# Performance work log

Measured on AMD Instinct MI355X. Metric: run time of the kernel, lower is better.

The kernel has to match this reference:

```python
import jax, jax.numpy as jnp
import numpy as np

N_NODES = 100000
N_EDGES = 3200000
R0, R1, R2, N1 = 16, 8, 16, 32


def setup_inputs() -> dict:
    key = jax.random.key(0)
    ks = jax.random.split(key, 12)
    x = jax.random.normal(ks[0], (N_NODES, R0), dtype=jnp.float32)
    edge_index = jax.random.randint(ks[1], (2, N_EDGES), 0, N_NODES, dtype=jnp.int64)
    s = 0.1
    return {
        "x": x,
        "edge_index": edge_index,
        # GraphConv 1: lin_rel (weight+bias) applied to aggregated neighbors, lin_root (no bias) to self
        "W_rel1": jax.random.normal(ks[2], (R0, R1), dtype=jnp.float32) * s,
        "b_rel1": jnp.zeros((R1,), dtype=jnp.float32),
        "W_root1": jax.random.normal(ks[3], (R0, R1), dtype=jnp.float32) * s,
        # GraphConv 2
        "W_rel2": jax.random.normal(ks[4], (R1, R2), dtype=jnp.float32) * s,
        "b_rel2": jnp.zeros((R2,), dtype=jnp.float32),
        "W_root2": jax.random.normal(ks[5], (R1, R2), dtype=jnp.float32) * s,
        # fc layers
        "W_fc1": jax.random.normal(ks[6], (R2, N1), dtype=jnp.float32) * s,
        "b_fc1": jnp.zeros((N1,), dtype=jnp.float32),
        "W_fc2": jax.random.normal(ks[7], (N1, 1), dtype=jnp.float32) * s,
        "b_fc2": jnp.zeros((1,), dtype=jnp.float32),
    }


def _graph_conv(x, src, dst, W_rel, b_rel, W_root):
    # GraphConv with aggr='add': out_i = lin_rel(sum_{j->i} x_j) + lin_root(x_i)
    agg = jax.ops.segment_sum(x[src], dst, num_segments=N_NODES)  # [N, d_in]
    return agg @ W_rel + b_rel + x @ W_root


def reference(x, edge_index,
              W_rel1, b_rel1, W_root1,
              W_rel2, b_rel2, W_root2,
              W_fc1, b_fc1, W_fc2, b_fc2):
    src, dst = edge_index[0], edge_index[1]
    h = jax.nn.relu(_graph_conv(x, src, dst, W_rel1, b_rel1, W_root1))
    h = jax.nn.relu(_graph_conv(h, src, dst, W_rel2, b_rel2, W_root2))
    h = jax.nn.relu(h @ W_fc1 + b_fc1)
    out = h @ W_fc2 + b_fc2  # [N, 1]
    return out - jnp.mean(out)
```

## Files before the change

### kernel.cpp

```cpp
#include <hip/hip_runtime.h>

#define NN 100000
#define NE 3200000
#define BSH 7
#define BNODES 128
#define NBUCK 782
#define BCAP 4800
#define BIN_CHUNK 8192
#define NBIN_BLOCKS ((NE + BIN_CHUNK - 1) / BIN_CHUNK)

#define S1 2097152.0f
#define S2 524288.0f
#define INV_S1 (1.0f / S1)
#define INV_S2 (1.0f / S2)

__global__ void node_layer1(const float* __restrict__ x,
                            const float* __restrict__ Wrel1,
                            const float* __restrict__ brel1,
                            const float* __restrict__ Wroot1,
                            int* __restrict__ y1q,
                            int* __restrict__ initq,
                            int* __restrict__ bucketCnt ) {
    __shared__ float sW[16 * 8];
    __shared__ float sR[16 * 8];
    __shared__ float sb[8];
    int t = threadIdx.x;
    if (t < 128) { sW[t] = Wrel1[t]; sR[t] = Wroot1[t]; }
    if (t < 8)   { sb[t] = brel1[t]; }
    if (blockIdx.x == 0) {
        for (int k = t; k < NBUCK + 1; k += 256) bucketCnt[k] = 0;
    }
    __syncthreads();

    int i = blockIdx.x * blockDim.x + t;
    if (i >= NN) return;

    const float4* xp = (const float4*)(x + (size_t)i * 16);
    float4 x0 = xp[0], x1 = xp[1], x2 = xp[2], x3 = xp[3];
    float xi[16] = {x0.x, x0.y, x0.z, x0.w, x1.x, x1.y, x1.z, x1.w,
                    x2.x, x2.y, x2.z, x2.w, x3.x, x3.y, x3.z, x3.w};

    float y[8], r[8];
#pragma unroll
    for (int j = 0; j < 8; ++j) { y[j] = 0.0f; r[j] = sb[j]; }
#pragma unroll
    for (int k = 0; k < 16; ++k) {
        float xv = xi[k];
#pragma unroll
        for (int j = 0; j < 8; ++j) {
            y[j] = fmaf(xv, sW[k * 8 + j], y[j]);
            r[j] = fmaf(xv, sR[k * 8 + j], r[j]);
        }
    }
    int4* yp = (int4*)(y1q + (size_t)i * 8);
    int4* ap = (int4*)(initq + (size_t)i * 8);
    int4 q0, q1, p0, p1;
    q0.x = __float2int_rn(y[0] * S1); q0.y = __float2int_rn(y[1] * S1);
    q0.z = __float2int_rn(y[2] * S1); q0.w = __float2int_rn(y[3] * S1);
    q1.x = __float2int_rn(y[4] * S1); q1.y = __float2int_rn(y[5] * S1);
    q1.z = __float2int_rn(y[6] * S1); q1.w = __float2int_rn(y[7] * S1);
    p0.x = __float2int_rn(r[0] * S1); p0.y = __float2int_rn(r[1] * S1);
    p0.z = __float2int_rn(r[2] * S1); p0.w = __float2int_rn(r[3] * S1);
    p1.x = __float2int_rn(r[4] * S1); p1.y = __float2int_rn(r[5] * S1);
    p1.z = __float2int_rn(r[6] * S1); p1.w = __float2int_rn(r[7] * S1);
    yp[0] = q0; yp[1] = q1;
    ap[0] = p0; ap[1] = p1;
}

__global__ __launch_bounds__(1024) void binning(const int* __restrict__ src,
                                                const int* __restrict__ dst,
                                                int* __restrict__ bucketCnt,
                                                int* __restrict__ bpay) {
    __shared__ int stage[BIN_CHUNK];
    __shared__ int hist[NBUCK];
    __shared__ int loff[NBUCK + 1];
    __shared__ int gbase[NBUCK];
    __shared__ int psum[1024];

    int t = threadIdx.x;
    int e0 = blockIdx.x * BIN_CHUNK;
    int nE = NE - e0; if (nE > BIN_CHUNK) nE = BIN_CHUNK;
    int nv = nE >> 2;

    if (t < NBUCK) hist[t] = 0;
    __syncthreads();

    const int4* dst4 = (const int4*)(dst + e0);
    const int4* src4 = (const int4*)(src + e0);

    for (int k = t; k < nv; k += 1024) {
        int4 d4 = dst4[k];
        atomicAdd(&hist[d4.x >> BSH], 1);
        atomicAdd(&hist[d4.y >> BSH], 1);
        atomicAdd(&hist[d4.z >> BSH], 1);
        atomicAdd(&hist[d4.w >> BSH], 1);
    }
    __syncthreads();

    int c = (t < NBUCK) ? hist[t] : 0;
    psum[t] = c;
    __syncthreads();
    for (int off = 1; off < 1024; off <<= 1) {
        int u = (t >= off) ? psum[t - off] : 0;
        __syncthreads();
        psum[t] += u;
        __syncthreads();
    }
    if (t < NBUCK) loff[t] = psum[t] - c;
    if (t == 0) loff[NBUCK] = nE;
    __syncthreads();

    if (t < NBUCK) {
        gbase[t] = c ? atomicAdd(&bucketCnt[t], c) : 0;
        hist[t] = loff[t];
    }
    __syncthreads();

    for (int k = t; k < nv; k += 1024) {
        int4 d4 = dst4[k];
        int4 s4 = src4[k];
        int b, r;
        b = d4.x >> BSH; r = atomicAdd(&hist[b], 1);
        stage[r] = ((d4.x & (BNODES - 1)) << 17) | s4.x;
        b = d4.y >> BSH; r = atomicAdd(&hist[b], 1);
        stage[r] = ((d4.y & (BNODES - 1)) << 17) | s4.y;
        b = d4.z >> BSH; r = atomicAdd(&hist[b], 1);
        stage[r] = ((d4.z & (BNODES - 1)) << 17) | s4.z;
        b = d4.w >> BSH; r = atomicAdd(&hist[b], 1);
        stage[r] = ((d4.w & (BNODES - 1)) << 17) | s4.w;
    }
    __syncthreads();

    for (int p = t; p < nE; p += 1024) {
        int lo = 0, hi = NBUCK - 1;
        while (lo < hi) {
            int mid = (lo + hi + 1) >> 1;
            if (loff[mid] <= p) lo = mid; else hi = mid - 1;
        }
        int ob = gbase[lo] + (p - loff[lo]);
        if (ob < BCAP) bpay[lo * BCAP + ob] = stage[p];
    }
}

__global__ __launch_bounds__(512, 6) void bucket_agg1(const int* __restrict__ bucketCnt,
                                                      const int* __restrict__ bpay,
                                                      const int* __restrict__ y1q,
                                                      int* __restrict__ h1q ) {
    __shared__ int qacc[BNODES * 8];
    int t = threadIdx.x;
    int b = blockIdx.x;
    int gb = b * BCAP;
    int fbase = b * (BNODES * 8);

    for (int k = t; k < BNODES * 8; k += 512) {
        int gi = fbase + k;
        qacc[k] = (gi < NN * 8) ? h1q[gi] : 0;
    }
    int C = bucketCnt[b]; if (C > BCAP) C = BCAP;
    __syncthreads();

    int f = t & 7, g = t >> 3;
    const int4* bp4 = (const int4*)(bpay + gb);
    int iters = C >> 9;
    for (int it = 0; it < iters; ++it) {
        int4 va = bp4[(it << 7) + (g << 1)];
        int4 vb = bp4[(it << 7) + (g << 1) + 1];
        int a0 = y1q[((va.x & 0x1FFFF) << 3) + f];
        int a1 = y1q[((va.y & 0x1FFFF) << 3) + f];
        int a2 = y1q[((va.z & 0x1FFFF) << 3) + f];
        int a3 = y1q[((va.w & 0x1FFFF) << 3) + f];
        int a4 = y1q[((vb.x & 0x1FFFF) << 3) + f];
        int a5 = y1q[((vb.y & 0x1FFFF) << 3) + f];
        int a6 = y1q[((vb.z & 0x1FFFF) << 3) + f];
        int a7 = y1q[((vb.w & 0x1FFFF) << 3) + f];
        atomicAdd(&qacc[((va.x >> 17) << 3) + f], a0);
        atomicAdd(&qacc[((va.y >> 17) << 3) + f], a1);
        atomicAdd(&qacc[((va.z >> 17) << 3) + f], a2);
        atomicAdd(&qacc[((va.w >> 17) << 3) + f], a3);
        atomicAdd(&qacc[((vb.x >> 17) << 3) + f], a4);
        atomicAdd(&qacc[((vb.y >> 17) << 3) + f], a5);
        atomicAdd(&qacc[((vb.z >> 17) << 3) + f], a6);
        atomicAdd(&qacc[((vb.w >> 17) << 3) + f], a7);
    }
    for (int e = (iters << 9) + g; e < C; e += 64) {
        int v = bpay[gb + e];
        int a = y1q[((v & 0x1FFFF) << 3) + f];
        atomicAdd(&qacc[((v >> 17) << 3) + f], a);
    }
    __syncthreads();

    for (int k = t; k < BNODES * 8; k += 512) {
        int gi = fbase + k;
        if (gi < NN * 8) {
            float h = (float)qacc[k] * INV_S1;
            h = h > 0.0f ? h : 0.0f;
            h1q[gi] = __float2int_rn(h * S2);
        }
    }
}

__global__ __launch_bounds__(512, 6) void bucket_agg2_tail(const int* __restrict__ bucketCnt,
                                                           const int* __restrict__ bpay,
                                                           const int* __restrict__ h1q,
                                                           const float* __restrict__ Wrel2,
                                                           const float* __restrict__ brel2,
                                                           const float* __restrict__ Wroot2,
                                                           const float* __restrict__ Wfc1,
                                                           const float* __restrict__ bfc1,
                                                           const float* __restrict__ Wfc2,
                                                           const float* __restrict__ bfc2,
                                                           float* __restrict__ out,
                                                           float* __restrict__ gsum) {
    __shared__ int qacc[BNODES * 8];
    __shared__ float sWrel2[128], sWroot2[128], sbrel2[16];
    __shared__ float sWfc1[512], sbfc1[32], sWfc2[32];
    __shared__ float sbfc2;
    __shared__ float wsum[8];

    int t = threadIdx.x;
    int b = blockIdx.x;
    int gb = b * BCAP;
    int n0 = b * BNODES;

    for (int k = t; k < BNODES * 8; k += 512) qacc[k] = 0;
    sWfc1[t] = Wfc1[t];
    if (t < 128) { sWrel2[t] = Wrel2[t]; sWroot2[t] = Wroot2[t]; }
    if (t >= 128 && t < 144) sbrel2[t - 128] = brel2[t - 128];
    if (t >= 192 && t < 224) { sbfc1[t - 192] = bfc1[t - 192]; sWfc2[t - 192] = Wfc2[t - 192]; }
    if (t == 256) sbfc2 = bfc2[0];
    int C = bucketCnt[b]; if (C > BCAP) C = BCAP;
    __syncthreads();

    int f = t & 7, g = t >> 3;
    const int4* bp4 = (const int4*)(bpay + gb);
    int iters = C >> 9;
    for (int it = 0; it < iters; ++it) {
        int4 va = bp4[(it << 7) + (g << 1)];
        int4 vb = bp4[(it << 7) + (g << 1) + 1];
        int a0 = h1q[((va.x & 0x1FFFF) << 3) + f];
        int a1 = h1q[((va.y & 0x1FFFF) << 3) + f];
        int a2 = h1q[((va.z & 0x1FFFF) << 3) + f];
        int a3 = h1q[((va.w & 0x1FFFF) << 3) + f];
        int a4 = h1q[((vb.x & 0x1FFFF) << 3) + f];
        int a5 = h1q[((vb.y & 0x1FFFF) << 3) + f];
        int a6 = h1q[((vb.z & 0x1FFFF) << 3) + f];
        int a7 = h1q[((vb.w & 0x1FFFF) << 3) + f];
        atomicAdd(&qacc[((va.x >> 17) << 3) + f], a0);
        atomicAdd(&qacc[((va.y >> 17) << 3) + f], a1);
        atomicAdd(&qacc[((va.z >> 17) << 3) + f], a2);
        atomicAdd(&qacc[((va.w >> 17) << 3) + f], a3);
        atomicAdd(&qacc[((vb.x >> 17) << 3) + f], a4);
        atomicAdd(&qacc[((vb.y >> 17) << 3) + f], a5);
        atomicAdd(&qacc[((vb.z >> 17) << 3) + f], a6);
        atomicAdd(&qacc[((vb.w >> 17) << 3) + f], a7);
    }
    for (int e = (iters << 9) + g; e < C; e += 64) {
        int v = bpay[gb + e];
        int a = h1q[((v & 0x1FFFF) << 3) + f];
        atomicAdd(&qacc[((v >> 17) << 3) + f], a);
    }
    __syncthreads();

    float o = 0.0f;
    int node = n0 + t;
    if (t < BNODES && node < NN) {
        const int4* hp = (const int4*)(h1q + (size_t)node * 8);
        int4 ha = hp[0], hb = hp[1];
        float h1v[8] = {ha.x * INV_S2, ha.y * INV_S2, ha.z * INV_S2, ha.w * INV_S2,
                        hb.x * INV_S2, hb.y * INV_S2, hb.z * INV_S2, hb.w * INV_S2};
        float s2[8];
#pragma unroll
        for (int j = 0; j < 8; ++j) s2[j] = (float)qacc[t * 8 + j] * INV_S2;

        float h2[16];
#pragma unroll
        for (int j = 0; j < 16; ++j) h2[j] = sbrel2[j];
#pragma unroll
        for (int k = 0; k < 8; ++k) {
            float sv = s2[k], hv = h1v[k];
#pragma unroll
            for (int j = 0; j < 16; ++j) {
                h2[j] = fmaf(sv, sWrel2[k * 16 + j], h2[j]);
                h2[j] = fmaf(hv, sWroot2[k * 16 + j], h2[j]);
            }
        }
#pragma unroll
        for (int j = 0; j < 16; ++j) h2[j] = h2[j] > 0.0f ? h2[j] : 0.0f;

        o = sbfc2;
#pragma unroll
        for (int m = 0; m < 32; ++m) {
            float a = sbfc1[m];
#pragma unroll
            for (int j = 0; j < 16; ++j) a = fmaf(h2[j], sWfc1[j * 32 + m], a);
            a = a > 0.0f ? a : 0.0f;
            o = fmaf(a, sWfc2[m], o);
        }
        out[node] = o;
    }

    float v = o;
#pragma unroll
    for (int off = 32; off > 0; off >>= 1) v += __shfl_down(v, off);
    int lane = t & 63, w = t >> 6;
    if (lane == 0) wsum[w] = v;
    __syncthreads();
    if (t == 0) {
        float s = 0.0f;
#pragma unroll
        for (int k = 0; k < 8; ++k) s += wsum[k];
        atomicAdd(gsum, s);
    }
}

__global__ void subtract_mean(float* __restrict__ out,
                              const float* __restrict__ gsum) {
    int i = blockIdx.x * blockDim.x + threadIdx.x;
    if (i < NN) out[i] -= (*gsum) * (1.0f / (float)NN);
}

extern "C" void kernel_launch(void* const* d_in, const int* in_sizes, int n_in,
                              void* d_out, int out_size, void* d_ws, size_t ws_size,
                              hipStream_t stream) {
    const float* x      = (const float*)d_in[0];
    const int*   ei     = (const int*)d_in[1];
    const float* Wrel1  = (const float*)d_in[2];
    const float* brel1  = (const float*)d_in[3];
    const float* Wroot1 = (const float*)d_in[4];
    const float* Wrel2  = (const float*)d_in[5];
    const float* brel2  = (const float*)d_in[6];
    const float* Wroot2 = (const float*)d_in[7];
    const float* Wfc1   = (const float*)d_in[8];
    const float* bfc1   = (const float*)d_in[9];
    const float* Wfc2   = (const float*)d_in[10];
    const float* bfc2   = (const float*)d_in[11];
    float* out = (float*)d_out;
    float* ws  = (float*)d_ws;

    int*   y1q       = (int*)ws;
    int*   h1q       = (int*)(ws + 800000);
    int*   bucketCnt = (int*)(ws + 1600000);
    float* gsum      = ws + 1600782;
    int*   bpay      = (int*)(ws + 1600783);

    const int* src = ei;
    const int* dst = ei + NE;

    node_layer1<<<(NN + 255) / 256, 256, 0, stream>>>(x, Wrel1, brel1, Wroot1,
                                                      y1q, h1q, bucketCnt);
    binning<<<NBIN_BLOCKS, 1024, 0, stream>>>(src, dst, bucketCnt, bpay);
    bucket_agg1<<<NBUCK, 512, 0, stream>>>(bucketCnt, bpay, y1q, h1q);
    bucket_agg2_tail<<<NBUCK, 512, 0, stream>>>(bucketCnt, bpay, h1q,
                                                Wrel2, brel2, Wroot2,
                                                Wfc1, bfc1, Wfc2, bfc2, out, gsum);
    subtract_mean<<<(NN + 255) / 256, 256, 0, stream>>>(out, gsum);
}
```

Baseline: 181.8 us.

## Fuse all GCN stages into one cooperative persistent kernel with grid syncs

After: 329.4 us. 81.2% more time.

```diff
diff --git a/kernel.cpp b/kernel.cpp
--- a/kernel.cpp
+++ b/kernel.cpp
@@ -1,4 +1,7 @@
 #include <hip/hip_runtime.h>
+#include <hip/hip_cooperative_groups.h>
+
+namespace cg = cooperative_groups;
 
 #define NN 100000
 #define NE 3200000
@@ -6,317 +9,308 @@
 #define BNODES 128
 #define NBUCK 782
 #define BCAP 4800
-#define BIN_CHUNK 8192
-#define NBIN_BLOCKS ((NE + BIN_CHUNK - 1) / BIN_CHUNK)
+#define NBLOCKS 256
+#define NTHREADS 1024
+#define CHUNK 12500
 
 #define S1 2097152.0f
 #define S2 524288.0f
 #define INV_S1 (1.0f / S1)
 #define INV_S2 (1.0f / S2)
 
-__global__ void node_layer1(const float* __restrict__ x,
-                            const float* __restrict__ Wrel1,
-                            const float* __restrict__ brel1,
-                            const float* __restrict__ Wroot1,
-                            int* __restrict__ y1q,
-                            int* __restrict__ initq,
-                            int* __restrict__ bucketCnt ) {
-    __shared__ float sW[16 * 8];
-    __shared__ float sR[16 * 8];
-    __shared__ float sb[8];
+struct BinSh {
+    int stage[CHUNK];
+    int hist[NBUCK];
+    int loff[NBUCK + 1];
+    int gbase[NBUCK];
+    int psum[NTHREADS];
+};
+struct ASh { float sW[128], sR[128], sb[8]; };
+struct AggSh {
+    int qacc[BNODES * 8];
+    float sWrel2[128], sWroot2[128], sbrel2[16];
+    float sWfc1[512], sbfc1[32], sWfc2[32], sbfc2;
+    float wsum[16];
+};
+union Sh { ASh a; BinSh bin; AggSh agg; };
+
+__global__ __launch_bounds__(NTHREADS, 4) void fused_gcn(
+    const float* __restrict__ x,
+    const int* __restrict__ src,
+    const int* __restrict__ dst,
+    const float* __restrict__ Wrel1, const float* __restrict__ brel1,
+    const float* __restrict__ Wroot1,
+    const float* __restrict__ Wrel2, const float* __restrict__ brel2,
+    const float* __restrict__ Wroot2,
+    const float* __restrict__ Wfc1, const float* __restrict__ bfc1,
+    const float* __restrict__ Wfc2, const float* __restrict__ bfc2,
+    int* __restrict__ y1q, int* __restrict__ h1q,
+    int* __restrict__ bucketCnt, float* __restrict__ gsum,
+    int* __restrict__ bpay, float* __restrict__ out)
+{
+    cg::grid_group grid = cg::this_grid();
+    __shared__ Sh sh;
     int t = threadIdx.x;
-    if (t < 128) { sW[t] = Wrel1[t]; sR[t] = Wroot1[t]; }
-    if (t < 8)   { sb[t] = brel1[t]; }
-    if (blockIdx.x == 0) {
-        for (int k = t; k < NBUCK + 1; k += 256) bucketCnt[k] = 0;
+    int blk = blockIdx.x;
+
+    if (t < 128) { sh.a.sW[t] = Wrel1[t]; sh.a.sR[t] = Wroot1[t]; }
+    if (t < 8)   sh.a.sb[t] = brel1[t];
+    if (blk == 0) {
+        for (int k = t; k < NBUCK; k += NTHREADS) bucketCnt[k] = 0;
+        if (t == 0) *gsum = 0.0f;
     }
     __syncthreads();
 
-    int i = blockIdx.x * blockDim.x + t;
-    if (i >= NN) return;
-
-    const float4* xp = (const float4*)(x + (size_t)i * 16);
-    float4 x0 = xp[0], x1 = xp[1], x2 = xp[2], x3 = xp[3];
-    float xi[16] = {x0.x, x0.y, x0.z, x0.w, x1.x, x1.y, x1.z, x1.w,
-                    x2.x, x2.y, x2.z, x2.w, x3.x, x3.y, x3.z, x3.w};
-
-    float y[8], r[8];
-#pragma unroll
-    for (int j = 0; j < 8; ++j) { y[j] = 0.0f; r[j] = sb[j]; }
-#pragma unroll
-    for (int k = 0; k < 16; ++k) {
-        float xv = xi[k];
-#pragma unroll
-        for (int j = 0; j < 8; ++j) {
-            y[j] = fmaf(xv, sW[k * 8 + j], y[j]);
-            r[j] = fmaf(xv, sR[k * 8 + j], r[j]);
-        }
-    }
-    int4* yp = (int4*)(y1q + (size_t)i * 8);
-    int4* ap = (int4*)(initq + (size_t)i * 8);
-    int4 q0, q1, p0, p1;
-    q0.x = __float2int_rn(y[0] * S1); q0.y = __float2int_rn(y[1] * S1);
-    q0.z = __float2int_rn(y[2] * S1); q0.w = __float2int_rn(y[3] * S1);
-    q1.x = __float2int_rn(y[4] * S1); q1.y = __float2int_rn(y[5] * S1);
-    q1.z = __float2int_rn(y[6] * S1); q1.w = __float2int_rn(y[7] * S1);
-    p0.x = __float2int_rn(r[0] * S1); p0.y = __float2int_rn(r[1] * S1);
-    p0.z = __float2int_rn(r[2] * S1); p0.w = __float2int_rn(r[3] * S1);
-    p1.x = __float2int_rn(r[4] * S1); p1.y = __float2int_rn(r[5] * S1);
-    p1.z = __float2int_rn(r[6] * S1); p1.w = __float2int_rn(r[7] * S1);
-    yp[0] = q0; yp[1] = q1;
-    ap[0] = p0; ap[1] = p1;
-}
-
-__global__ __launch_bounds__(1024) void binning(const int* __restrict__ src,
-                                                const int* __restrict__ dst,
-                                                int* __restrict__ bucketCnt,
-                                                int* __restrict__ bpay) {
-    __shared__ int stage[BIN_CHUNK];
-    __shared__ int hist[NBUCK];
-    __shared__ int loff[NBUCK + 1];
-    __shared__ int gbase[NBUCK];
-    __shared__ int psum[1024];
-
-    int t = threadIdx.x;
-    int e0 = blockIdx.x * BIN_CHUNK;
-    int nE = NE - e0; if (nE > BIN_CHUNK) nE = BIN_CHUNK;
-    int nv = nE >> 2;
-
-    if (t < NBUCK) hist[t] = 0;
+    int i = blk * NTHREADS + t;
+    if (i < NN) {
+        const float4* xp = (const float4*)(x + (size_t)i * 16);
+        float4 x0 = xp[0], x1 = xp[1], x2 = xp[2], x3 = xp[3];
+        float xi[16] = {x0.x, x0.y, x0.z, x0.w, x1.x, x1.y, x1.z, x1.w,
+                        x2.x, x2.y, x2.z, x2.w, x3.x, x3.y, x3.z, x3.w};
+        float y[8], r[8];
+#pragma unroll
+        for (int j = 0; j < 8; ++j) { y[j] = 0.0f; r[j] = sh.a.sb[j]; }
+#pragma unroll
+        for (int k = 0; k < 16; ++k) {
+            float xv = xi[k];
+#pragma unroll
+            for (int j = 0; j < 8; ++j) {
+                y[j] = fmaf(xv, sh.a.sW[k * 8 + j], y[j]);
+                r[j] = fmaf(xv, sh.a.sR[k * 8 + j], r[j]);
+            }
+        }
+        int4* yp = (int4*)(y1q + (size_t)i * 8);
+        int4* ap = (int4*)(h1q + (size_t)i * 8);
+        int4 q0, q1, p0, p1;
+        q0.x = __float2int_rn(y[0] * S1); q0.y = __float2int_rn(y[1] * S1);
+        q0.z = __float2int_rn(y[2] * S1); q0.w = __float2int_rn(y[3] * S1);
+        q1.x = __float2int_rn(y[4] * S1); q1.y = __float2int_rn(y[5] * S1);
+        q1.z = __float2int_rn(y[6] * S1); q1.w = __float2int_rn(y[7] * S1);
+        p0.x = __float2int_rn(r[0] * S1); p0.y = __float2int_rn(r[1] * S1);
+        p0.z = __float2int_rn(r[2] * S1); p0.w = __float2int_rn(r[3] * S1);
+        p1.x = __float2int_rn(r[4] * S1); p1.y = __float2int_rn(r[5] * S1);
+        p1.z = __float2int_rn(r[6] * S1); p1.w = __float2int_rn(r[7] * S1);
+        yp[0] = q0; yp[1] = q1;
+        ap[0] = p0; ap[1] = p1;
+    }
     __syncthreads();
-
-    const int4* dst4 = (const int4*)(dst + e0);
-    const int4* src4 = (const int4*)(src + e0);
-
-    for (int k = t; k < nv; k += 1024) {
-        int4 d4 = dst4[k];
-        atomicAdd(&hist[d4.x >> BSH], 1);
-        atomicAdd(&hist[d4.y >> BSH], 1);
-        atomicAdd(&hist[d4.z >> BSH], 1);
-        atomicAdd(&hist[d4.w >> BSH], 1);
-    }
-    __syncthreads();
-
-    int c = (t < NBUCK) ? hist[t] : 0;
-    psum[t] = c;
-    __syncthreads();
-    for (int off = 1; off < 1024; off <<= 1) {
-        int u = (t >= off) ? psum[t - off] : 0;
-        __syncthreads();
-        psum[t] += u;
-        __syncthreads();
-    }
-    if (t < NBUCK) loff[t] = psum[t] - c;
-    if (t == 0) loff[NBUCK] = nE;
-    __syncthreads();
-
-    if (t < NBUCK) {
-        gbase[t] = c ? atomicAdd(&bucketCnt[t], c) : 0;
-        hist[t] = loff[t];
-    }
-    __syncthreads();
-
-    for (int k = t; k < nv; k += 1024) {
-        int4 d4 = dst4[k];
-        int4 s4 = src4[k];
-        int b, r;
-        b = d4.x >> BSH; r = atomicAdd(&hist[b], 1);
-        stage[r] = ((d4.x & (BNODES - 1)) << 17) | s4.x;
-        b = d4.y >> BSH; r = atomicAdd(&hist[b], 1);
-        stage[r] = ((d4.y & (BNODES - 1)) << 17) | s4.y;
-        b = d4.z >> BSH; r = atomicAdd(&hist[b], 1);
-        stage[r] = ((d4.z & (BNODES - 1)) << 17) | s4.z;
-        b = d4.w >> BSH; r = atomicAdd(&hist[b], 1);
-        stage[r] = ((d4.w & (BNODES - 1)) << 17) | s4.w;
-    }
-    __syncthreads();
-
-    for (int p = t; p < nE; p += 1024) {
-        int lo = 0, hi = NBUCK - 1;
-        while (lo < hi) {
-            int mid = (lo + hi + 1) >> 1;
-            if (loff[mid] <= p) lo = mid; else hi = mid - 1;
-        }
-        int ob = gbase[lo] + (p - loff[lo]);
-        if (ob < BCAP) bpay[lo * BCAP + ob] = stage[p];
-    }
-}
-
-__global__ __launch_bounds__(512, 6) void bucket_agg1(const int* __restrict__ bucketCnt,
-                                                      const int* __restrict__ bpay,
-                                                      const int* __restrict__ y1q,
-                                                      int* __restrict__ h1q ) {
-    __shared__ int qacc[BNODES * 8];
-    int t = threadIdx.x;
-    int b = blockIdx.x;
-    int gb = b * BCAP;
-    int fbase = b * (BNODES * 8);
-
-    for (int k = t; k < BNODES * 8; k += 512) {
-        int gi = fbase + k;
-        qacc[k] = (gi < NN * 8) ? h1q[gi] : 0;
-    }
-    int C = bucketCnt[b]; if (C > BCAP) C = BCAP;
-    __syncthreads();
+    grid.sync();
+
+    {
+        int e0 = blk * CHUNK;
+        const int4* dst4 = (const int4*)(dst + e0);
+        const int4* src4 = (const int4*)(src + e0);
+
+        for (int k = t; k < NBUCK; k += NTHREADS) sh.bin.hist[k] = 0;
+        __syncthreads();
+
+        for (int k = t; k < CHUNK / 4; k += NTHREADS) {
+            int4 d4 = dst4[k];
+            atomicAdd(&sh.bin.hist[d4.x >> BSH], 1);
+            atomicAdd(&sh.bin.hist[d4.y >> BSH], 1);
+            atomicAdd(&sh.bin.hist[d4.z >> BSH], 1);
+            atomicAdd(&sh.bin.hist[d4.w >> BSH], 1);
+        }
+        __syncthreads();
+
+        int c = (t < NBUCK) ? sh.bin.hist[t] : 0;
+        sh.bin.psum[t] = c;
+        __syncthreads();
+        for (int off = 1; off < NTHREADS; off <<= 1) {
+            int u = (t >= off) ? sh.bin.psum[t - off] : 0;
+            __syncthreads();
+            sh.bin.psum[t] += u;
+            __syncthreads();
+        }
+        if (t < NBUCK) sh.bin.loff[t] = sh.bin.psum[t] - c;
+        if (t == 0) sh.bin.loff[NBUCK] = CHUNK;
+        __syncthreads();
+
+        if (t < NBUCK) {
+            sh.bin.gbase[t] = c ? atomicAdd(&bucketCnt[t], c) : 0;
+            sh.bin.hist[t] = sh.bin.loff[t];
+        }
+        __syncthreads();
+
+        for (int k = t; k < CHUNK / 4; k += NTHREADS) {
+            int4 d4 = dst4[k];
+            int4 s4 = src4[k];
+            int b, r;
+            b = d4.x >> BSH; r = atomicAdd(&sh.bin.hist[b], 1);
+            sh.bin.stage[r] = ((d4.x & (BNODES - 1)) << 17) | s4.x;
+            b = d4.y >> BSH; r = atomicAdd(&sh.bin.hist[b], 1);
+            sh.bin.stage[r] = ((d4.y & (BNODES - 1)) << 17) | s4.y;
+            b = d4.z >> BSH; r = atomicAdd(&sh.bin.hist[b], 1);
+            sh.bin.stage[r] = ((d4.z & (BNODES - 1)) << 17) | s4.z;
+            b = d4.w >> BSH; r = atomicAdd(&sh.bin.hist[b], 1);
+            sh.bin.stage[r] = ((d4.w & (BNODES - 1)) << 17) | s4.w;
+        }
+        __syncthreads();
+
+        for (int p = t; p < CHUNK; p += NTHREADS) {
+            int lo = 0, hi = NBUCK - 1;
+            while (lo < hi) {
+                int mid = (lo + hi + 1) >> 1;
+                if (sh.bin.loff[mid] <= p) lo = mid; else hi = mid - 1;
+            }
+            int ob = sh.bin.gbase[lo] + (p - sh.bin.loff[lo]);
+            if (ob < BCAP) bpay[lo * BCAP + ob] = sh.bin.stage[p];
+        }
+    }
+    grid.sync();
 
     int f = t & 7, g = t >> 3;
-    const int4* bp4 = (const int4*)(bpay + gb);
-    int iters = C >> 9;
-    for (int it = 0; it < iters; ++it) {
-        int4 va = bp4[(it << 7) + (g << 1)];
-        int4 vb = bp4[(it << 7) + (g << 1) + 1];
-        int a0 = y1q[((va.x & 0x1FFFF) << 3) + f];
-        int a1 = y1q[((va.y & 0x1FFFF) << 3) + f];
-        int a2 = y1q[((va.z & 0x1FFFF) << 3) + f];
-        int a3 = y1q[((va.w & 0x1FFFF) << 3) + f];
-        int a4 = y1q[((vb.x & 0x1FFFF) << 3) + f];
-        int a5 = y1q[((vb.y & 0x1FFFF) << 3) + f];
-        int a6 = y1q[((vb.z & 0x1FFFF) << 3) + f];
-        int a7 = y1q[((vb.w & 0x1FFFF) << 3) + f];
-        atomicAdd(&qacc[((va.x >> 17) << 3) + f], a0);
-        atomicAdd(&qacc[((va.y >> 17) << 3) + f], a1);
-        atomicAdd(&qacc[((va.z >> 17) << 3) + f], a2);
-        atomicAdd(&qacc[((va.w >> 17) << 3) + f], a3);
-        atomicAdd(&qacc[((vb.x >> 17) << 3) + f], a4);
-        atomicAdd(&qacc[((vb.y >> 17) << 3) + f], a5);
-        atomicAdd(&qacc[((vb.z >> 17) << 3) + f], a6);
-        atomicAdd(&qacc[((vb.w >> 17) << 3) + f], a7);
-    }
-    for (int e = (iters << 9) + g; e < C; e += 64) {
-        int v = bpay[gb + e];
-        int a = y1q[((v & 0x1FFFF) << 3) + f];
-        atomicAdd(&qacc[((v >> 17) << 3) + f], a);
-    }
-    __syncthreads();
-
-    for (int k = t; k < BNODES * 8; k += 512) {
-        int gi = fbase + k;
-        if (gi < NN * 8) {
-            float h = (float)qacc[k] * INV_S1;
-            h = h > 0.0f ? h : 0.0f;
-            h1q[gi] = __float2int_rn(h * S2);
-        }
-    }
-}
-
-__global__ __launch_bounds__(512, 6) void bucket_agg2_tail(const int* __restrict__ bucketCnt,
-                                                           const int* __restrict__ bpay,
-                                                           const int* __restrict__ h1q,
-                                                           const float* __restrict__ Wrel2,
-                                                           const float* __restrict__ brel2,
-                                                           const float* __restrict__ Wroot2,
-                                                           const float* __restrict__ Wfc1,
-                                                           const float* __restrict__ bfc1,
-                                                           const float* __restrict__ Wfc2,
-                                                           const float* __restrict__ bfc2,
-                                                           float* __restrict__ out,
-                                                           float* __restrict__ gsum) {
-    __shared__ int qacc[BNODES * 8];
-    __shared__ float sWrel2[128], sWroot2[128], sbrel2[16];
-    __shared__ float sWfc1[512], sbfc1[32], sWfc2[32];
-    __shared__ float sbfc2;
-    __shared__ float wsum[8];
-
-    int t = threadIdx.x;
-    int b = blockIdx.x;
-    int gb = b * BCAP;
-    int n0 = b * BNODES;
-
-    for (int k = t; k < BNODES * 8; k += 512) qacc[k] = 0;
-    sWfc1[t] = Wfc1[t];
-    if (t < 128) { sWrel2[t] = Wrel2[t]; sWroot2[t] = Wroot2[t]; }
-    if (t >= 128 && t < 144) sbrel2[t - 128] = brel2[t - 128];
-    if (t >= 192 && t < 224) { sbfc1[t - 192] = bfc1[t - 192]; sWfc2[t - 192] = Wfc2[t - 192]; }
-    if (t == 256) sbfc2 = bfc2[0];
-    int C = bucketCnt[b]; if (C > BCAP) C = BCAP;
-    __syncthreads();
-
-    int f = t & 7, g = t >> 3;
-    const int4* bp4 = (const int4*)(bpay + gb);
-    int iters = C >> 9;
-    for (int it = 0; it < iters; ++it) {
-        int4 va = bp4[(it << 7) + (g << 1)];
-        int4 vb = bp4[(it << 7) + (g << 1) + 1];
-        int a0 = h1q[((va.x & 0x1FFFF) << 3) + f];
-        int a1 = h1q[((va.y & 0x1FFFF) << 3) + f];
-        int a2 = h1q[((va.z & 0x1FFFF) << 3) + f];
-        int a3 = h1q[((va.w & 0x1FFFF) << 3) + f];
-        int a4 = h1q[((vb.x & 0x1FFFF) << 3) + f];
-        int a5 = h1q[((vb.y & 0x1FFFF) << 3) + f];
-        int a6 = h1q[((vb.z & 0x1FFFF) << 3) + f];
-        int a7 = h1q[((vb.w & 0x1FFFF) << 3) + f];
-        atomicAdd(&qacc[((va.x >> 17) << 3) + f], a0);
-        atomicAdd(&qacc[((va.y >> 17) << 3) + f], a1);
-        atomicAdd(&qacc[((va.z >> 17) << 3) + f], a2);
-        atomicAdd(&qacc[((va.w >> 17) << 3) + f], a3);
-        atomicAdd(&qacc[((vb.x >> 17) << 3) + f], a4);
-        atomicAdd(&qacc[((vb.y >> 17) << 3) + f], a5);
-        atomicAdd(&qacc[((vb.z >> 17) << 3) + f], a6);
-        atomicAdd(&qacc[((vb.w >> 17) << 3) + f], a7);
-    }
-    for (int e = (iters << 9) + g; e < C; e += 64) {
-        int v = bpay[gb + e];
-        int a = h1q[((v & 0x1FFFF) << 3) + f];
-        atomicAdd(&qacc[((v >> 17) << 3) + f], a);
-    }
-    __syncthreads();
-
-    float o = 0.0f;
-    int node = n0 + t;
-    if (t < BNODES && node < NN) {
-        const int4* hp = (const int4*)(h1q + (size_t)node * 8);
-        int4 ha = hp[0], hb = hp[1];
-        float h1v[8] = {ha.x * INV_S2, ha.y * INV_S2, ha.z * INV_S2, ha.w * INV_S2,
-                        hb.x * INV_S2, hb.y * INV_S2, hb.z * INV_S2, hb.w * INV_S2};
-        float s2[8];
-#pragma unroll
-        for (int j = 0; j < 8; ++j) s2[j] = (float)qacc[t * 8 + j] * INV_S2;
-
-        float h2[16];
-#pragma unroll
-        for (int j = 0; j < 16; ++j) h2[j] = sbrel2[j];
-#pragma unroll
-        for (int k = 0; k < 8; ++k) {
-            float sv = s2[k], hv = h1v[k];
-#pragma unroll
-            for (int j = 0; j < 16; ++j) {
-                h2[j] = fmaf(sv, sWrel2[k * 16 + j], h2[j]);
-                h2[j] = fmaf(hv, sWroot2[k * 16 + j], h2[j]);
-            }
-        }
-#pragma unroll
-        for (int j = 0; j < 16; ++j) h2[j] = h2[j] > 0.0f ? h2[j] : 0.0f;
-
-        o = sbfc2;
-#pragma unroll
-        for (int m = 0; m < 32; ++m) {
-            float a = sbfc1[m];
-#pragma unroll
-            for (int j = 0; j < 16; ++j) a = fmaf(h2[j], sWfc1[j * 32 + m], a);
-            a = a > 0.0f ? a : 0.0f;
-            o = fmaf(a, sWfc2[m], o);
-        }
-        out[node] = o;
-    }
-
-    float v = o;
-#pragma unroll
-    for (int off = 32; off > 0; off >>= 1) v += __shfl_down(v, off);
-    int lane = t & 63, w = t >> 6;
-    if (lane == 0) wsum[w] = v;
-    __syncthreads();
-    if (t == 0) {
-        float s = 0.0f;
-#pragma unroll
-        for (int k = 0; k < 8; ++k) s += wsum[k];
-        atomicAdd(gsum, s);
-    }
-}
-
-__global__ void subtract_mean(float* __restrict__ out,
-                              const float* __restrict__ gsum) {
-    int i = blockIdx.x * blockDim.x + threadIdx.x;
-    if (i < NN) out[i] -= (*gsum) * (1.0f / (float)NN);
+    for (int b = blk; b < NBUCK; b += NBLOCKS) {
+        int gb = b * BCAP;
+        int fbase = b * (BNODES * 8);
+        __syncthreads();
+        for (int k = t; k < BNODES * 8; k += NTHREADS) {
+            int gi = fbase + k;
+            sh.agg.qacc[k] = (gi < NN * 8) ? h1q[gi] : 0;
+        }
+        int C = bucketCnt[b]; if (C > BCAP) C = BCAP;
+        __syncthreads();
+
+        const int4* bp4 = (const int4*)(bpay + gb);
+        int iters = C >> 10;
+        for (int it = 0; it < iters; ++it) {
+            int4 va = bp4[(it << 8) + (g << 1)];
+            int4 vb = bp4[(it << 8) + (g << 1) + 1];
+            int a0 = y1q[((va.x & 0x1FFFF) << 3) + f];
+            int a1 = y1q[((va.y & 0x1FFFF) << 3) + f];
+            int a2 = y1q[((va.z & 0x1FFFF) << 3) + f];
+            int a3 = y1q[((va.w & 0x1FFFF) << 3) + f];
+            int a4 = y1q[((vb.x & 0x1FFFF) << 3) + f];
+            int a5 = y1q[((vb.y & 0x1FFFF) << 3) + f];
+            int a6 = y1q[((vb.z & 0x1FFFF) << 3) + f];
+            int a7 = y1q[((vb.w & 0x1FFFF) << 3) + f];
+            atomicAdd(&sh.agg.qacc[((va.x >> 17) << 3) + f], a0);
+            atomicAdd(&sh.agg.qacc[((va.y >> 17) << 3) + f], a1);
+            atomicAdd(&sh.agg.qacc[((va.z >> 17) << 3) + f], a2);
+            atomicAdd(&sh.agg.qacc[((va.w >> 17) << 3) + f], a3);
+            atomicAdd(&sh.agg.qacc[((vb.x >> 17) << 3) + f], a4);
+            atomicAdd(&sh.agg.qacc[((vb.y >> 17) << 3) + f], a5);
+            atomicAdd(&sh.agg.qacc[((vb.z >> 17) << 3) + f], a6);
+            atomicAdd(&sh.agg.qacc[((vb.w >> 17) << 3) + f], a7);
+        }
+        for (int e = (iters << 10) + g; e < C; e += 128) {
+            int v = bpay[gb + e];
+            int a = y1q[((v & 0x1FFFF) << 3) + f];
+            atomicAdd(&sh.agg.qacc[((v >> 17) << 3) + f], a);
+        }
+        __syncthreads();
+
+        for (int k = t; k < BNODES * 8; k += NTHREADS) {
+            int gi = fbase + k;
+            if (gi < NN * 8) {
+                float h = (float)sh.agg.qacc[k] * INV_S1;
+                h = h > 0.0f ? h : 0.0f;
+                h1q[gi] = __float2int_rn(h * S2);
+            }
+        }
+    }
+    grid.sync();
+
+    if (t < 512) sh.agg.sWfc1[t] = Wfc1[t];
+    if (t < 128) { sh.agg.sWrel2[t] = Wrel2[t]; sh.agg.sWroot2[t] = Wroot2[t]; }
+    if (t < 16)  sh.agg.sbrel2[t] = brel2[t];
+    if (t < 32)  { sh.agg.sbfc1[t] = bfc1[t]; sh.agg.sWfc2[t] = Wfc2[t]; }
+    if (t == 0)  sh.agg.sbfc2 = bfc2[0];
+
+    for (int b = blk; b < NBUCK; b += NBLOCKS) {
+        int gb = b * BCAP;
+        int n0 = b * BNODES;
+        __syncthreads();
+        for (int k = t; k < BNODES * 8; k += NTHREADS) sh.agg.qacc[k] = 0;
+        int C = bucketCnt[b]; if (C > BCAP) C = BCAP;
+        __syncthreads();
+
+        const int4* bp4 = (const int4*)(bpay + gb);
+        int iters = C >> 10;
+        for (int it = 0; it < iters; ++it) {
+            int4 va = bp4[(it << 8) + (g << 1)];
+            int4 vb = bp4[(it << 8) + (g << 1) + 1];
+            int a0 = h1q[((va.x & 0x1FFFF) << 3) + f];
+            int a1 = h1q[((va.y & 0x1FFFF) << 3) + f];
+            int a2 = h1q[((va.z & 0x1FFFF) << 3) + f];
+            int a3 = h1q[((va.w & 0x1FFFF) << 3) + f];
+            int a4 = h1q[((vb.x & 0x1FFFF) << 3) + f];
+            int a5 = h1q[((vb.y & 0x1FFFF) << 3) + f];
+            int a6 = h1q[((vb.z & 0x1FFFF) << 3) + f];
+            int a7 = h1q[((vb.w & 0x1FFFF) << 3) + f];
+            atomicAdd(&sh.agg.qacc[((va.x >> 17) << 3) + f], a0);
+            atomicAdd(&sh.agg.qacc[((va.y >> 17) << 3) + f], a1);
+            atomicAdd(&sh.agg.qacc[((va.z >> 17) << 3) + f], a2);
+            atomicAdd(&sh.agg.qacc[((va.w >> 17) << 3) + f], a3);
+            atomicAdd(&sh.agg.qacc[((vb.x >> 17) << 3) + f], a4);
+            atomicAdd(&sh.agg.qacc[((vb.y >> 17) << 3) + f], a5);
+            atomicAdd(&sh.agg.qacc[((vb.z >> 17) << 3) + f], a6);
+            atomicAdd(&sh.agg.qacc[((vb.w >> 17) << 3) + f], a7);
+        }
+        for (int e = (iters << 10) + g; e < C; e += 128) {
+            int v = bpay[gb + e];
+            int a = h1q[((v & 0x1FFFF) << 3) + f];
+            atomicAdd(&sh.agg.qacc[((v >> 17) << 3) + f], a);
+        }
+        __syncthreads();
+
+        float o = 0.0f;
+        int node = n0 + t;
+        if (t < BNODES && node < NN) {
+            const int4* hp = (const int4*)(h1q + (size_t)node * 8);
+            int4 ha = hp[0], hb = hp[1];
+            float h1v[8] = {ha.x * INV_S2, ha.y * INV_S2, ha.z * INV_S2, ha.w * INV_S2,
+                            hb.x * INV_S2, hb.y * INV_S2, hb.z * INV_S2, hb.w * INV_S2};
+            float s2[8];
+#pragma unroll
+            for (int j = 0; j < 8; ++j) s2[j] = (float)sh.agg.qacc[t * 8 + j] * INV_S2;
+
+            float h2[16];
+#pragma unroll
+            for (int j = 0; j < 16; ++j) h2[j] = sh.agg.sbrel2[j];
+#pragma unroll
+            for (int k = 0; k < 8; ++k) {
+                float sv = s2[k], hv = h1v[k];
+#pragma unroll
+                for (int j = 0; j < 16; ++j) {
+                    h2[j] = fmaf(sv, sh.agg.sWrel2[k * 16 + j], h2[j]);
+                    h2[j] = fmaf(hv, sh.agg.sWroot2[k * 16 + j], h2[j]);
+                }
+            }
+#pragma unroll
+            for (int j = 0; j < 16; ++j) h2[j] = h2[j] > 0.0f ? h2[j] : 0.0f;
+
+            o = sh.agg.sbfc2;
+#pragma unroll
+            for (int m = 0; m < 32; ++m) {
+                float a = sh.agg.sbfc1[m];
+#pragma unroll
+                for (int j = 0; j < 16; ++j) a = fmaf(h2[j], sh.agg.sWfc1[j * 32 + m], a);
+                a = a > 0.0f ? a : 0.0f;
+                o = fmaf(a, sh.agg.sWfc2[m], o);
+            }
+            out[node] = o;
+        }
+
+        float v = o;
+#pragma unroll
+        for (int off = 32; off > 0; off >>= 1) v += __shfl_down(v, off);
+        int lane = t & 63, w = t >> 6;
+        if (lane == 0) sh.agg.wsum[w] = v;
+        __syncthreads();
+        if (t == 0) {
+            float s = 0.0f;
+#pragma unroll
+            for (int k = 0; k < 16; ++k) s += sh.agg.wsum[k];
+            atomicAdd(gsum, s);
+        }
+    }
+    grid.sync();
+
+    float m = __hip_atomic_load(gsum, __ATOMIC_RELAXED, __HIP_MEMORY_SCOPE_AGENT)
+              * (1.0f / (float)NN);
+    for (int k = blk * NTHREADS + t; k < NN; k += NBLOCKS * NTHREADS)
+        out[k] -= m;
 }
 
 extern "C" void kernel_launch(void* const* d_in, const int* in_sizes, int n_in,
@@ -337,21 +331,23 @@
     float* out = (float*)d_out;
     float* ws  = (float*)d_ws;
 
+    const int* src = ei;
+    const int* dst = ei + NE;
+
     int*   y1q       = (int*)ws;
     int*   h1q       = (int*)(ws + 800000);
     int*   bucketCnt = (int*)(ws + 1600000);
     float* gsum      = ws + 1600782;
     int*   bpay      = (int*)(ws + 1600783);
 
-    const int* src = ei;
-    const int* dst = ei + NE;
-
-    node_layer1<<<(NN + 255) / 256, 256, 0, stream>>>(x, Wrel1, brel1, Wroot1,
-                                                      y1q, h1q, bucketCnt);
-    binning<<<NBIN_BLOCKS, 1024, 0, stream>>>(src, dst, bucketCnt, bpay);
-    bucket_agg1<<<NBUCK, 512, 0, stream>>>(bucketCnt, bpay, y1q, h1q);
-    bucket_agg2_tail<<<NBUCK, 512, 0, stream>>>(bucketCnt, bpay, h1q,
-                                                Wrel2, brel2, Wroot2,
-                                                Wfc1, bfc1, Wfc2, bfc2, out, gsum);
-    subtract_mean<<<(NN + 255) / 256, 256, 0, stream>>>(out, gsum);
+    void* args[] = {
+        (void*)&x, (void*)&src, (void*)&dst,
+        (void*)&Wrel1, (void*)&brel1, (void*)&Wroot1,
+        (void*)&Wrel2, (void*)&brel2, (void*)&Wroot2,
+        (void*)&Wfc1, (void*)&bfc1, (void*)&Wfc2, (void*)&bfc2,
+        (void*)&y1q, (void*)&h1q, (void*)&bucketCnt, (void*)&gsum,
+        (void*)&bpay, (void*)&out,
+    };
+    hipLaunchCooperativeKernel((void*)fused_gcn, dim3(NBLOCKS), dim3(NTHREADS),
+                               args, 0, stream);
 }
```

## Fuse layer1 into binning, stage bucket indices in LDS, fold mean subtraction

Applied to the files above, without the earlier changes.

Result: slower. 195.1 us (+7.3%).

```diff
diff --git a/kernel.cpp b/kernel.cpp
--- a/kernel.cpp
+++ b/kernel.cpp
@@ -8,81 +8,85 @@
 #define BCAP 4800
 #define BIN_CHUNK 8192
 #define NBIN_BLOCKS ((NE + BIN_CHUNK - 1) / BIN_CHUNK)
+#define NL1_BLOCKS ((NN + 1023) / 1024)
+#define SUB_BLOCKS 64
+#define SUB_RANGE ((NN + SUB_BLOCKS - 1) / SUB_BLOCKS)
 
 #define S1 2097152.0f
 #define S2 524288.0f
 #define INV_S1 (1.0f / S1)
 #define INV_S2 (1.0f / S2)
 
-__global__ void node_layer1(const float* __restrict__ x,
-                            const float* __restrict__ Wrel1,
-                            const float* __restrict__ brel1,
-                            const float* __restrict__ Wroot1,
-                            int* __restrict__ y1q,
-                            int* __restrict__ initq,
-                            int* __restrict__ bucketCnt ) {
-    __shared__ float sW[16 * 8];
-    __shared__ float sR[16 * 8];
-    __shared__ float sb[8];
+__global__ void init_ws(int* __restrict__ p) {
     int t = threadIdx.x;
-    if (t < 128) { sW[t] = Wrel1[t]; sR[t] = Wroot1[t]; }
-    if (t < 8)   { sb[t] = brel1[t]; }
-    if (blockIdx.x == 0) {
-        for (int k = t; k < NBUCK + 1; k += 256) bucketCnt[k] = 0;
-    }
-    __syncthreads();
-
-    int i = blockIdx.x * blockDim.x + t;
-    if (i >= NN) return;
-
-    const float4* xp = (const float4*)(x + (size_t)i * 16);
-    float4 x0 = xp[0], x1 = xp[1], x2 = xp[2], x3 = xp[3];
-    float xi[16] = {x0.x, x0.y, x0.z, x0.w, x1.x, x1.y, x1.z, x1.w,
-                    x2.x, x2.y, x2.z, x2.w, x3.x, x3.y, x3.z, x3.w};
-
-    float y[8], r[8];
-#pragma unroll
-    for (int j = 0; j < 8; ++j) { y[j] = 0.0f; r[j] = sb[j]; }
-#pragma unroll
-    for (int k = 0; k < 16; ++k) {
-        float xv = xi[k];
-#pragma unroll
-        for (int j = 0; j < 8; ++j) {
-            y[j] = fmaf(xv, sW[k * 8 + j], y[j]);
-            r[j] = fmaf(xv, sR[k * 8 + j], r[j]);
-        }
-    }
-    int4* yp = (int4*)(y1q + (size_t)i * 8);
-    int4* ap = (int4*)(initq + (size_t)i * 8);
-    int4 q0, q1, p0, p1;
-    q0.x = __float2int_rn(y[0] * S1); q0.y = __float2int_rn(y[1] * S1);
-    q0.z = __float2int_rn(y[2] * S1); q0.w = __float2int_rn(y[3] * S1);
-    q1.x = __float2int_rn(y[4] * S1); q1.y = __float2int_rn(y[5] * S1);
-    q1.z = __float2int_rn(y[6] * S1); q1.w = __float2int_rn(y[7] * S1);
-    p0.x = __float2int_rn(r[0] * S1); p0.y = __float2int_rn(r[1] * S1);
-    p0.z = __float2int_rn(r[2] * S1); p0.w = __float2int_rn(r[3] * S1);
-    p1.x = __float2int_rn(r[4] * S1); p1.y = __float2int_rn(r[5] * S1);
-    p1.z = __float2int_rn(r[6] * S1); p1.w = __float2int_rn(r[7] * S1);
-    yp[0] = q0; yp[1] = q1;
-    ap[0] = p0; ap[1] = p1;
-}
-
-__global__ __launch_bounds__(1024) void binning(const int* __restrict__ src,
-                                                const int* __restrict__ dst,
-                                                int* __restrict__ bucketCnt,
-                                                int* __restrict__ bpay) {
-    __shared__ int stage[BIN_CHUNK];
-    __shared__ int hist[NBUCK];
-    __shared__ int loff[NBUCK + 1];
-    __shared__ int gbase[NBUCK];
-    __shared__ int psum[1024];
-
+    if (t < NBUCK + 2) p[t] = 0;
+}
+
+struct BinSh {
+    int stage[BIN_CHUNK];
+    int hist[NBUCK];
+    int loff[NBUCK + 1];
+    int gbase[NBUCK];
+    int psum[1024];
+};
+struct L1Sh { float sW[128], sR[128], sb[8]; };
+union K1Sh { BinSh bin; L1Sh a; };
+
+__global__ __launch_bounds__(1024) void layer1_bin(
+    const float* __restrict__ x,
+    const int* __restrict__ src, const int* __restrict__ dst,
+    const float* __restrict__ Wrel1, const float* __restrict__ brel1,
+    const float* __restrict__ Wroot1,
+    int* __restrict__ y1q, int* __restrict__ initq,
+    int* __restrict__ bucketCnt, int* __restrict__ bpay)
+{
+    __shared__ K1Sh sh;
     int t = threadIdx.x;
-    int e0 = blockIdx.x * BIN_CHUNK;
+    int blk = blockIdx.x;
+
+    if (blk >= NBIN_BLOCKS) {
+        if (t < 128) { sh.a.sW[t] = Wrel1[t]; sh.a.sR[t] = Wroot1[t]; }
+        if (t < 8)   sh.a.sb[t] = brel1[t];
+        __syncthreads();
+        int i = (blk - NBIN_BLOCKS) * 1024 + t;
+        if (i >= NN) return;
+        const float4* xp = (const float4*)(x + (size_t)i * 16);
+        float4 x0 = xp[0], x1 = xp[1], x2 = xp[2], x3 = xp[3];
+        float xi[16] = {x0.x, x0.y, x0.z, x0.w, x1.x, x1.y, x1.z, x1.w,
+                        x2.x, x2.y, x2.z, x2.w, x3.x, x3.y, x3.z, x3.w};
+        float y[8], r[8];
+#pragma unroll
+        for (int j = 0; j < 8; ++j) { y[j] = 0.0f; r[j] = sh.a.sb[j]; }
+#pragma unroll
+        for (int k = 0; k < 16; ++k) {
+            float xv = xi[k];
+#pragma unroll
+            for (int j = 0; j < 8; ++j) {
+                y[j] = fmaf(xv, sh.a.sW[k * 8 + j], y[j]);
+                r[j] = fmaf(xv, sh.a.sR[k * 8 + j], r[j]);
+            }
+        }
+        int4* yp = (int4*)(y1q + (size_t)i * 8);
+        int4* ap = (int4*)(initq + (size_t)i * 8);
+        int4 q0, q1, p0, p1;
+        q0.x = __float2int_rn(y[0] * S1); q0.y = __float2int_rn(y[1] * S1);
+        q0.z = __float2int_rn(y[2] * S1); q0.w = __float2int_rn(y[3] * S1);
+        q1.x = __float2int_rn(y[4] * S1); q1.y = __float2int_rn(y[5] * S1);
+        q1.z = __float2int_rn(y[6] * S1); q1.w = __float2int_rn(y[7] * S1);
+        p0.x = __float2int_rn(r[0] * S1); p0.y = __float2int_rn(r[1] * S1);
+        p0.z = __float2int_rn(r[2] * S1); p0.w = __float2int_rn(r[3] * S1);
+        p1.x = __float2int_rn(r[4] * S1); p1.y = __float2int_rn(r[5] * S1);
+        p1.z = __float2int_rn(r[6] * S1); p1.w = __float2int_rn(r[7] * S1);
+        yp[0] = q0; yp[1] = q1;
+        ap[0] = p0; ap[1] = p1;
+        return;
+    }
+
+    int e0 = blk * BIN_CHUNK;
     int nE = NE - e0; if (nE > BIN_CHUNK) nE = BIN_CHUNK;
     int nv = nE >> 2;
 
-    if (t < NBUCK) hist[t] = 0;
+    if (t < NBUCK) sh.bin.hist[t] = 0;
     __syncthreads();
 
     const int4* dst4 = (const int4*)(dst + e0);
@@ -90,29 +94,29 @@
 
     for (int k = t; k < nv; k += 1024) {
         int4 d4 = dst4[k];
-        atomicAdd(&hist[d4.x >> BSH], 1);
-        atomicAdd(&hist[d4.y >> BSH], 1);
-        atomicAdd(&hist[d4.z >> BSH], 1);
-        atomicAdd(&hist[d4.w >> BSH], 1);
-    }
-    __syncthreads();
-
-    int c = (t < NBUCK) ? hist[t] : 0;
-    psum[t] = c;
+        atomicAdd(&sh.bin.hist[d4.x >> BSH], 1);
+        atomicAdd(&sh.bin.hist[d4.y >> BSH], 1);
+        atomicAdd(&sh.bin.hist[d4.z >> BSH], 1);
+        atomicAdd(&sh.bin.hist[d4.w >> BSH], 1);
+    }
+    __syncthreads();
+
+    int c = (t < NBUCK) ? sh.bin.hist[t] : 0;
+    sh.bin.psum[t] = c;
     __syncthreads();
     for (int off = 1; off < 1024; off <<= 1) {
-        int u = (t >= off) ? psum[t - off] : 0;
+        int u = (t >= off) ? sh.bin.psum[t - off] : 0;
         __syncthreads();
-        psum[t] += u;
+        sh.bin.psum[t] += u;
         __syncthreads();
     }
-    if (t < NBUCK) loff[t] = psum[t] - c;
-    if (t == 0) loff[NBUCK] = nE;
+    if (t < NBUCK) sh.bin.loff[t] = sh.bin.psum[t] - c;
+    if (t == 0) sh.bin.loff[NBUCK] = nE;
     __syncthreads();
 
     if (t < NBUCK) {
-        gbase[t] = c ? atomicAdd(&bucketCnt[t], c) : 0;
-        hist[t] = loff[t];
+        sh.bin.gbase[t] = c ? atomicAdd(&bucketCnt[t], c) : 0;
+        sh.bin.hist[t] = sh.bin.loff[t];
     }
     __syncthreads();
 
@@ -120,14 +124,14 @@
         int4 d4 = dst4[k];
         int4 s4 = src4[k];
         int b, r;
-        b = d4.x >> BSH; r = atomicAdd(&hist[b], 1);
-        stage[r] = ((d4.x & (BNODES - 1)) << 17) | s4.x;
-        b = d4.y >> BSH; r = atomicAdd(&hist[b], 1);
-        stage[r] = ((d4.y & (BNODES - 1)) << 17) | s4.y;
-        b = d4.z >> BSH; r = atomicAdd(&hist[b], 1);
-        stage[r] = ((d4.z & (BNODES - 1)) << 17) | s4.z;
-        b = d4.w >> BSH; r = atomicAdd(&hist[b], 1);
-        stage[r] = ((d4.w & (BNODES - 1)) << 17) | s4.w;
+        b = d4.x >> BSH; r = atomicAdd(&sh.bin.hist[b], 1);
+        sh.bin.stage[r] = ((d4.x & (BNODES - 1)) << 17) | s4.x;
+        b = d4.y >> BSH; r = atomicAdd(&sh.bin.hist[b], 1);
+        sh.bin.stage[r] = ((d4.y & (BNODES - 1)) << 17) | s4.y;
+        b = d4.z >> BSH; r = atomicAdd(&sh.bin.hist[b], 1);
+        sh.bin.stage[r] = ((d4.z & (BNODES - 1)) << 17) | s4.z;
+        b = d4.w >> BSH; r = atomicAdd(&sh.bin.hist[b], 1);
+        sh.bin.stage[r] = ((d4.w & (BNODES - 1)) << 17) | s4.w;
     }
     __syncthreads();
 
@@ -135,36 +139,41 @@
         int lo = 0, hi = NBUCK - 1;
         while (lo < hi) {
             int mid = (lo + hi + 1) >> 1;
-            if (loff[mid] <= p) lo = mid; else hi = mid - 1;
-        }
-        int ob = gbase[lo] + (p - loff[lo]);
-        if (ob < BCAP) bpay[lo * BCAP + ob] = stage[p];
-    }
-}
-
-__global__ __launch_bounds__(512, 6) void bucket_agg1(const int* __restrict__ bucketCnt,
+            if (sh.bin.loff[mid] <= p) lo = mid; else hi = mid - 1;
+        }
+        int ob = sh.bin.gbase[lo] + (p - sh.bin.loff[lo]);
+        if (ob < BCAP) bpay[lo * BCAP + ob] = sh.bin.stage[p];
+    }
+}
+
+__global__ __launch_bounds__(512, 8) void bucket_agg1(const int* __restrict__ bucketCnt,
                                                       const int* __restrict__ bpay,
                                                       const int* __restrict__ y1q,
                                                       int* __restrict__ h1q ) {
+    __shared__ int4 sidx4[BCAP / 4];
     __shared__ int qacc[BNODES * 8];
     int t = threadIdx.x;
     int b = blockIdx.x;
     int gb = b * BCAP;
     int fbase = b * (BNODES * 8);
 
+    int C = bucketCnt[b]; if (C > BCAP) C = BCAP;
+    const int4* bp4 = (const int4*)(bpay + gb);
+    int C4 = (C + 3) >> 2;
+    for (int k = t; k < C4; k += 512) sidx4[k] = bp4[k];
     for (int k = t; k < BNODES * 8; k += 512) {
         int gi = fbase + k;
         qacc[k] = (gi < NN * 8) ? h1q[gi] : 0;
     }
-    int C = bucketCnt[b]; if (C > BCAP) C = BCAP;
     __syncthreads();
 
     int f = t & 7, g = t >> 3;
-    const int4* bp4 = (const int4*)(bpay + gb);
-    int iters = C >> 9;
-    for (int it = 0; it < iters; ++it) {
-        int4 va = bp4[(it << 7) + (g << 1)];
-        int4 vb = bp4[(it << 7) + (g << 1) + 1];
+    const int* sidx = (const int*)sidx4;
+    int full = C >> 9;
+    for (int it = 0; it < full; ++it) {
+        int base4 = (it << 7) + (g << 1);
+        int4 va = sidx4[base4];
+        int4 vb = sidx4[base4 + 1];
         int a0 = y1q[((va.x & 0x1FFFF) << 3) + f];
         int a1 = y1q[((va.y & 0x1FFFF) << 3) + f];
         int a2 = y1q[((va.z & 0x1FFFF) << 3) + f];
@@ -182,8 +191,8 @@
         atomicAdd(&qacc[((vb.z >> 17) << 3) + f], a6);
         atomicAdd(&qacc[((vb.w >> 17) << 3) + f], a7);
     }
-    for (int e = (iters << 9) + g; e < C; e += 64) {
-        int v = bpay[gb + e];
+    for (int e = (full << 9) + g; e < C; e += 64) {
+        int v = sidx[e];
         int a = y1q[((v & 0x1FFFF) << 3) + f];
         atomicAdd(&qacc[((v >> 17) << 3) + f], a);
     }
@@ -199,44 +208,48 @@
     }
 }
 
-__global__ __launch_bounds__(512, 6) void bucket_agg2_tail(const int* __restrict__ bucketCnt,
-                                                           const int* __restrict__ bpay,
-                                                           const int* __restrict__ h1q,
-                                                           const float* __restrict__ Wrel2,
-                                                           const float* __restrict__ brel2,
-                                                           const float* __restrict__ Wroot2,
-                                                           const float* __restrict__ Wfc1,
-                                                           const float* __restrict__ bfc1,
-                                                           const float* __restrict__ Wfc2,
-                                                           const float* __restrict__ bfc2,
-                                                           float* __restrict__ out,
-                                                           float* __restrict__ gsum) {
+__global__ __launch_bounds__(512, 8) void bucket_agg2_tail_sub(
+    const int* __restrict__ bucketCnt,
+    const int* __restrict__ bpay,
+    const int* __restrict__ h1q,
+    const float* __restrict__ Wrel2, const float* __restrict__ brel2,
+    const float* __restrict__ Wroot2,
+    const float* __restrict__ Wfc1, const float* __restrict__ bfc1,
+    const float* __restrict__ Wfc2, const float* __restrict__ bfc2,
+    float* __restrict__ out, float* __restrict__ gsum, int* __restrict__ done)
+{
+    __shared__ int4 sidx4[BCAP / 4];
     __shared__ int qacc[BNODES * 8];
     __shared__ float sWrel2[128], sWroot2[128], sbrel2[16];
     __shared__ float sWfc1[512], sbfc1[32], sWfc2[32];
     __shared__ float sbfc2;
     __shared__ float wsum[8];
+    __shared__ int sticket;
 
     int t = threadIdx.x;
     int b = blockIdx.x;
     int gb = b * BCAP;
     int n0 = b * BNODES;
 
+    int C = bucketCnt[b]; if (C > BCAP) C = BCAP;
+    const int4* bp4 = (const int4*)(bpay + gb);
+    int C4 = (C + 3) >> 2;
+    for (int k = t; k < C4; k += 512) sidx4[k] = bp4[k];
     for (int k = t; k < BNODES * 8; k += 512) qacc[k] = 0;
     sWfc1[t] = Wfc1[t];
     if (t < 128) { sWrel2[t] = Wrel2[t]; sWroot2[t] = Wroot2[t]; }
     if (t >= 128 && t < 144) sbrel2[t - 128] = brel2[t - 128];
     if (t >= 192 && t < 224) { sbfc1[t - 192] = bfc1[t - 192]; sWfc2[t - 192] = Wfc2[t - 192]; }
     if (t == 256) sbfc2 = bfc2[0];
-    int C = bucketCnt[b]; if (C > BCAP) C = BCAP;
     __syncthreads();
 
     int f = t & 7, g = t >> 3;
-    const int4* bp4 = (const int4*)(bpay + gb);
-    int iters = C >> 9;
-    for (int it = 0; it < iters; ++it) {
-        int4 va = bp4[(it << 7) + (g << 1)];
-        int4 vb = bp4[(it << 7) + (g << 1) + 1];
+    const int* sidx = (const int*)sidx4;
+    int full = C >> 9;
+    for (int it = 0; it < full; ++it) {
+        int base4 = (it << 7) + (g << 1);
+        int4 va = sidx4[base4];
+        int4 vb = sidx4[base4 + 1];
         int a0 = h1q[((va.x & 0x1FFFF) << 3) + f];
         int a1 = h1q[((va.y & 0x1FFFF) << 3) + f];
         int a2 = h1q[((va.z & 0x1FFFF) << 3) + f];
@@ -254,8 +267,8 @@
         atomicAdd(&qacc[((vb.z >> 17) << 3) + f], a6);
         atomicAdd(&qacc[((vb.w >> 17) << 3) + f], a7);
     }
-    for (int e = (iters << 9) + g; e < C; e += 64) {
-        int v = bpay[gb + e];
+    for (int e = (full << 9) + g; e < C; e += 64) {
+        int v = sidx[e];
         int a = h1q[((v & 0x1FFFF) << 3) + f];
         atomicAdd(&qacc[((v >> 17) << 3) + f], a);
     }
@@ -310,13 +323,24 @@
 #pragma unroll
         for (int k = 0; k < 8; ++k) s += wsum[k];
         atomicAdd(gsum, s);
-    }
-}
-
-__global__ void subtract_mean(float* __restrict__ out,
-                              const float* __restrict__ gsum) {
-    int i = blockIdx.x * blockDim.x + threadIdx.x;
-    if (i < NN) out[i] -= (*gsum) * (1.0f / (float)NN);
+        __threadfence();
+        sticket = atomicAdd(done, 1);
+    }
+    __syncthreads();
+
+    int ticket = sticket;
+    if (ticket < NBUCK - SUB_BLOCKS) return;
+
+    if (t == 0) {
+        while (__hip_atomic_load(done, __ATOMIC_ACQUIRE, __HIP_MEMORY_SCOPE_AGENT) < NBUCK) {}
+    }
+    __syncthreads();
+    float m = __hip_atomic_load(gsum, __ATOMIC_RELAXED, __HIP_MEMORY_SCOPE_AGENT)
+              * (1.0f / (float)NN);
+    int r = ticket - (NBUCK - SUB_BLOCKS);
+    int s0 = r * SUB_RANGE;
+    int s1 = s0 + SUB_RANGE; if (s1 > NN) s1 = NN;
+    for (int i = s0 + t; i < s1; i += 512) out[i] -= m;
 }
 
 extern "C" void kernel_launch(void* const* d_in, const int* in_sizes, int n_in,
@@ -341,17 +365,18 @@
     int*   h1q       = (int*)(ws + 800000);
     int*   bucketCnt = (int*)(ws + 1600000);
     float* gsum      = ws + 1600782;
-    int*   bpay      = (int*)(ws + 1600783);
+    int*   done      = (int*)(ws + 1600783);
+    int*   bpay      = (int*)(ws + 1600784);
 
     const int* src = ei;
     const int* dst = ei + NE;
 
-    node_layer1<<<(NN + 255) / 256, 256, 0, stream>>>(x, Wrel1, brel1, Wroot1,
-                                                      y1q, h1q, bucketCnt);
-    binning<<<NBIN_BLOCKS, 1024, 0, stream>>>(src, dst, bucketCnt, bpay);
+    init_ws<<<1, 1024, 0, stream>>>(bucketCnt);
+    layer1_bin<<<NBIN_BLOCKS + NL1_BLOCKS, 1024, 0, stream>>>(
+        x, src, dst, Wrel1, brel1, Wroot1, y1q, h1q, bucketCnt, bpay);
     bucket_agg1<<<NBUCK, 512, 0, stream>>>(bucketCnt, bpay, y1q, h1q);
-    bucket_agg2_tail<<<NBUCK, 512, 0, stream>>>(bucketCnt, bpay, h1q,
-                                                Wrel2, brel2, Wroot2,
-                                                Wfc1, bfc1, Wfc2, bfc2, out, gsum);
-    subtract_mean<<<(NN + 255) / 256, 256, 0, stream>>>(out, gsum);
-}
+    bucket_agg2_tail_sub<<<NBUCK, 512, 0, stream>>>(bucketCnt, bpay, h1q,
+                                                    Wrel2, brel2, Wroot2,
+                                                    Wfc1, bfc1, Wfc2, bfc2,
+                                                    out, gsum, done);
+}
```
